# Optimization experiments

Hardware: AMD Instinct MI355X
Metric: run time of the kernel (lower is better)

The kernel has to match this reference:

```python
import jax, jax.numpy as jnp
import numpy as np
import math

IMAGE_SIZE = 256
VIEWING_ANGLE = 30.0  # degrees
NEAR = 0.1
FAR = 100.0
CHUNK = 50


def _look_at(vertices):
    # nr.look_at with at=origin, up=+y, eye from viewing_angle (as in __init__)
    eye = jnp.array([0.0, 0.0, -(1.0 / math.tan(math.radians(VIEWING_ANGLE)) + 1.0)],
                    dtype=vertices.dtype)
    at = jnp.zeros(3, dtype=vertices.dtype)
    up = jnp.array([0.0, 1.0, 0.0], dtype=vertices.dtype)
    z = at - eye
    z = z / jnp.linalg.norm(z)
    x = jnp.cross(up, z)
    x = x / jnp.linalg.norm(x)
    y = jnp.cross(z, x)
    y = y / jnp.linalg.norm(y)
    R = jnp.stack([x, y, z])  # [3,3] rows = camera axes
    return (vertices - eye) @ R.T


def _perspective(v):
    # nr.perspective: x,y divided by z*tan(angle); z (camera depth) kept
    width = math.tan(math.radians(VIEWING_ANGLE))
    z = v[..., 2]
    zs = jnp.where(jnp.abs(z) < 1e-5, 1e-5, z)  # avoid div-by-zero for behind-camera verts
    return jnp.stack([v[..., 0] / (zs * width), v[..., 1] / (zs * width), z], axis=-1)


def reference(vertices, faces):
    """Renderer.forward(vertices, faces, mode='depth'):
    fill_back -> look_at -> perspective -> vertices_to_faces -> rasterize_depth.
    Returns depth image [B, H, W] (FAR where no face covers the pixel)."""
    B = vertices.shape[0]
    # fill_back: append faces with reversed vertex order
    faces2 = jnp.concatenate([faces, faces[:, :, ::-1]], axis=1)  # [B, 2F, 3]
    v_scr = _perspective(_look_at(vertices))                      # [B, V, 3]
    # vertices_to_faces gather
    fv = jax.vmap(lambda v, f: v[f])(v_scr, faces2)               # [B, 2F, 3, 3]
    F2 = fv.shape[1]
    nsteps = F2 // CHUNK
    fv = fv.reshape(B, nsteps, CHUNK, 3, 3).transpose(1, 0, 2, 3, 4)  # [S,B,C,3,3]

    is_ = IMAGE_SIZE
    p = (2.0 * jnp.arange(is_, dtype=vertices.dtype) + 1.0 - is_) / is_  # pixel centers in (-1,1)
    py, px = jnp.meshgrid(p, p, indexing='ij')  # [H,W]

    def step(buf, f):  # f: [B,C,3,3]; z-buffer min over this face chunk
        x = f[..., 0][..., None, None]  # [B,C,3,1,1]
        y = f[..., 1][..., None, None]
        z = f[..., 2]                   # [B,C,3] camera-space depth per vertex
        x0, x1, x2 = x[:, :, 0], x[:, :, 1], x[:, :, 2]
        y0, y1, y2 = y[:, :, 0], y[:, :, 1], y[:, :, 2]
        area = (x1 - x0) * (y2 - y0) - (x2 - x0) * (y1 - y0)  # [B,C,1,1] signed 2*area
        area_s = jnp.where(jnp.abs(area) < 1e-8, 1e-8, area)
        # screen-space barycentric weights (edge functions / area)
        w0 = ((x1 - px) * (y2 - py) - (x2 - px) * (y1 - py)) / area_s
        w1 = ((x2 - px) * (y0 - py) - (x0 - px) * (y2 - py)) / area_s
        w2 = 1.0 - w0 - w1
        zc = jnp.maximum(z, 1e-4)  # safe for masked-out faces only
        # perspective-correct depth: z = 1 / (w0/z0 + w1/z1 + w2/z2)
        inv_z = (w0 / zc[:, :, 0, None, None] + w1 / zc[:, :, 1, None, None]
                 + w2 / zc[:, :, 2, None, None])
        zp = 1.0 / jnp.maximum(inv_z, 1e-6)
        front = jnp.all(z > NEAR, axis=-1)[..., None, None]
        inside = (w0 >= 0) & (w1 >= 0) & (w2 >= 0) & (jnp.abs(area) > 1e-8)
        valid = inside & front & (zp > NEAR) & (zp < FAR)
        zp = jnp.where(valid, zp, FAR)
        return jnp.minimum(buf, jnp.min(zp, axis=1)), None

    buf0 = jnp.full((B, is_, is_), FAR, dtype=vertices.dtype)
    depth, _ = jax.lax.scan(step, buf0, fv)
    return depth


def setup_inputs() -> dict:
    key = jax.random.key(0)
    kv, kf = jax.random.split(key)
    B, NV, NF = 1, 2502, 5000
    # mesh roughly within the camera frustum (eye at z~-2.73 looking at origin)
    vertices = 0.35 * jax.random.normal(kv, (B, NV, 3), dtype=jnp.float32)
    faces = jax.random.randint(kf, (B, NF, 3), 0, NV, dtype=jnp.int32)
    return {"vertices": vertices, "faces": faces}
```

## Files before the change

### kernel.cpp

```cpp
#include <hip/hip_runtime.h>

#define IS 256
#define NEARV 0.1f
#define FARV 100.0f
#define NTX 16
#define NTILES 256
#define SEGSZ 256
#define NSEGMAX 20
#define CAP (SEGSZ * NSEGMAX)
#define CHK 32
#define RBLOCKS 2048
#define RWAVES (RBLOCKS * 4)
#define NSLOTS (NTILES * 256)

__launch_bounds__(256)
__global__ void kprep(const float* __restrict__ verts, const int* __restrict__ faces,
                      float4* __restrict__ fd, int* __restrict__ cnt2,
                      unsigned short* __restrict__ list, unsigned int* __restrict__ zb,
                      int nf, int nseg) {
    __shared__ int scnt[NTILES];
    const int tid = threadIdx.x;
    const int bid = blockIdx.x;
    zb[bid * 256 + tid] = 0x42C80000u;
    if (bid >= nseg) return;

    scnt[tid] = 0;
    __syncthreads();

    const int f = bid * 256 + tid;
    int kx0 = 0, kx1 = -1, ky0 = 0, ky1 = -1;
    float bxmin = 0.f, bymin = 0.f, bxmax = -1.f, bymax = -1.f;
    if (f < nf) {
        int i0 = faces[f * 3 + 0];
        int i1 = faces[f * 3 + 1];
        int i2 = faces[f * 3 + 2];
        float z0 = verts[i0 * 3 + 2] + 2.7320508075688772f;
        float z1 = verts[i1 * 3 + 2] + 2.7320508075688772f;
        float z2 = verts[i2 * 3 + 2] + 2.7320508075688772f;
        bool front = (z0 > NEARV) && (z1 > NEARV) && (z2 > NEARV);
        float zs0 = (fabsf(z0) < 1e-5f) ? 1e-5f : z0;
        float zs1 = (fabsf(z1) < 1e-5f) ? 1e-5f : z1;
        float zs2 = (fabsf(z2) < 1e-5f) ? 1e-5f : z2;
        float d0 = zs0 * 0.57735026918962576f;
        float d1 = zs1 * 0.57735026918962576f;
        float d2 = zs2 * 0.57735026918962576f;
        float x0 = verts[i0 * 3 + 0] / d0;
        float y0 = verts[i0 * 3 + 1] / d0;
        float x1 = verts[i1 * 3 + 0] / d1;
        float y1 = verts[i1 * 3 + 1] / d1;
        float x2 = verts[i2 * 3 + 0] / d2;
        float y2 = verts[i2 * 3 + 1] / d2;
        float area = (x1 - x0) * (y2 - y0) - (x2 - x0) * (y1 - y0);
        if (front && (fabsf(area) > 1e-8f)) {
            bxmin = fminf(x0, fminf(x1, x2));
            bxmax = fmaxf(x0, fmaxf(x1, x2));
            bymin = fminf(y0, fminf(y1, y2));
            bymax = fmaxf(y0, fmaxf(y1, y2));
            float ia = 1.0f / area;
            float iz0 = 1.0f / fmaxf(z0, 1e-4f);
            float iz1 = 1.0f / fmaxf(z1, 1e-4f);
            float iz2 = 1.0f / fmaxf(z2, 1e-4f);
            float4* o = fd + (size_t)f * 4;
            o[0] = make_float4(x0, y0, x1, y1);
            o[1] = make_float4(x2, y2, ia, iz0);
            o[2] = make_float4(iz1, iz2, 0.0f, 0.0f);
            float tminx = fminf(fmaxf((bxmin * 256.0f + 225.0f) * (1.0f / 32.0f), -2.0f), 17.0f);
            float tmaxx = fminf(fmaxf((bxmax * 256.0f + 255.0f) * (1.0f / 32.0f), -2.0f), 17.0f);
            float tminy = fminf(fmaxf((bymin * 256.0f + 225.0f) * (1.0f / 32.0f), -2.0f), 17.0f);
            float tmaxy = fminf(fmaxf((bymax * 256.0f + 255.0f) * (1.0f / 32.0f), -2.0f), 17.0f);
            kx0 = max(0, (int)ceilf(tminx) - 1);
            kx1 = min(NTX - 1, (int)floorf(tmaxx) + 1);
            ky0 = max(0, (int)ceilf(tminy) - 1);
            ky1 = min(NTX - 1, (int)floorf(tmaxy) + 1);
        }
    }
    for (int ky = ky0; ky <= ky1; ++ky) {
        float py_lo = (float)(32 * ky - 255) * (1.0f / 256.0f);
        float py_hi = (float)(32 * ky - 225) * (1.0f / 256.0f);
        if (!(bymin <= py_hi && bymax >= py_lo)) continue;
        for (int kx = kx0; kx <= kx1; ++kx) {
            float px_lo = (float)(32 * kx - 255) * (1.0f / 256.0f);
            float px_hi = (float)(32 * kx - 225) * (1.0f / 256.0f);
            if (bxmin <= px_hi && bxmax >= px_lo) atomicAdd(&scnt[ky * NTX + kx], 1);
        }
    }
    __syncthreads();
    cnt2[tid * nseg + bid] = scnt[tid];
    scnt[tid] = 0;
    __syncthreads();
    for (int ky = ky0; ky <= ky1; ++ky) {
        float py_lo = (float)(32 * ky - 255) * (1.0f / 256.0f);
        float py_hi = (float)(32 * ky - 225) * (1.0f / 256.0f);
        if (!(bymin <= py_hi && bymax >= py_lo)) continue;
        for (int kx = kx0; kx <= kx1; ++kx) {
            float px_lo = (float)(32 * kx - 255) * (1.0f / 256.0f);
            float px_hi = (float)(32 * kx - 225) * (1.0f / 256.0f);
            if (bxmin <= px_hi && bxmax >= px_lo) {
                int t = ky * NTX + kx;
                int slot = atomicAdd(&scnt[t], 1);
                list[(size_t)t * CAP + bid * SEGSZ + slot] = (unsigned short)f;
            }
        }
    }
}

__launch_bounds__(256)
__global__ void kraster(const float4* __restrict__ fd, const unsigned short* __restrict__ list,
                        const int* __restrict__ cnt2, unsigned int* __restrict__ zb,
                        int nseg) {
    __shared__ float4 sdata[4][CHK * 3];
    const int wslot = __builtin_amdgcn_readfirstlane(threadIdx.x >> 6);
    const int wid = blockIdx.x * 4 + wslot;
    const int lane = threadIdx.x & 63;
    const int cx = lane & 15;
    const int ry = lane >> 4;
    float4* sd = &sdata[wslot][0];

    for (int w = wid; w < NSLOTS; w += RWAVES) {
        const int tile = w >> 8;
        const int slot = (w & 255) ^ tile;
        const int seg = slot >> 3;
        if (seg >= nseg) continue;
        const int c = cnt2[tile * nseg + seg];
        const int k = slot & 7;
        const int n0 = c - k * CHK;
        if (n0 <= 0) continue;
        const int n = min(CHK, n0);

        const int bx = tile & 15;
        const int by = tile >> 4;
        const int j = bx * 16 + cx;
        const float px = ((float)(2 * j + 1) - 256.0f) * (1.0f / 256.0f);
        float py[4];
        int row[4];
        unsigned int zcur[4];
#pragma unroll
        for (int r = 0; r < 4; ++r) {
            row[r] = by * 16 + ry + 4 * r;
            py[r] = ((float)(2 * row[r] + 1) - 256.0f) * (1.0f / 256.0f);
            zcur[r] = zb[row[r] * IS + j];
        }
        const unsigned short* lp = list + (size_t)tile * CAP + seg * SEGSZ + k * CHK;
        if (lane < n) {
            const int fidx = lp[lane];
            const float4* p = fd + (size_t)fidx * 4;
            float4 b0 = p[0];
            float4 b1 = p[1];
            float4 b2 = p[2];
            sd[lane * 3 + 0] = b0;
            sd[lane * 3 + 1] = b1;
            sd[lane * 3 + 2] = b2;
        }
        asm volatile("s_waitcnt lgkmcnt(0)" ::: "memory");

        float mx[4] = {0.0f, 0.0f, 0.0f, 0.0f};

#pragma unroll 2
        for (int e = 0; e < n; ++e) {
            float4 a0 = sd[e * 3 + 0];
            float4 a1 = sd[e * 3 + 1];
            float4 a2 = sd[e * 3 + 2];
            float dx0 = a0.x - px, dx1 = a0.z - px, dx2 = a1.x - px;
#pragma unroll
            for (int r = 0; r < 4; ++r) {
                float dy0 = a0.y - py[r], dy1 = a0.w - py[r], dy2 = a1.y - py[r];
                float e0 = dx1 * dy2 - dx2 * dy1;
                float e1 = dx2 * dy0 - dx0 * dy2;
                float w0 = e0 * a1.z;
                float w1 = e1 * a1.z;
                float w2 = 1.0f - w0 - w1;
                float invz = w0 * a1.w + w1 * a2.x + w2 * a2.y;
                float invzc = fmaxf(invz, 1e-6f);
                float wmin = fminf(fminf(w0, w1), w2);
                bool ok = (wmin >= 0.0f) && (invzc < 10.0f) && (invzc > 0.01f);
                if (ok) mx[r] = fmaxf(mx[r], invzc);
            }
        }
#pragma unroll
        for (int r = 0; r < 4; ++r) {
            if (mx[r] > 0.0f) {
                float zp = 1.0f / mx[r];
                unsigned int zbits = __float_as_uint(zp);
                if (zbits < zcur[r]) atomicMin(&zb[row[r] * IS + j], zbits);
            }
        }
    }
}

extern "C" void kernel_launch(void* const* d_in, const int* in_sizes, int n_in,
                              void* d_out, int out_size, void* d_ws, size_t ws_size,
                              hipStream_t stream) {
    const float* verts = (const float*)d_in[0];
    const int* faces = (const int*)d_in[1];
    unsigned int* zb = (unsigned int*)d_out;

    const int nf = in_sizes[1] / 3;
    const int nseg = (nf + SEGSZ - 1) / SEGSZ;

    char* ws = (char*)d_ws;
    size_t off = 0;
    float4* fd = (float4*)(ws + off);     off += (size_t)nf * 64;
    off = (off + 255) & ~(size_t)255;
    int* cnt2 = (int*)(ws + off);         off += (size_t)NTILES * NSEGMAX * 4;
    off = (off + 255) & ~(size_t)255;
    unsigned short* list = (unsigned short*)(ws + off);

    kprep<<<256, 256, 0, stream>>>(verts, faces, fd, cnt2, list, zb, nf, nseg);
    kraster<<<RBLOCKS, 256, 0, stream>>>(fd, list, cnt2, zb, nseg);
}
```

Baseline: 119.8 us.

## Use larger face segments and scrambled slot mapping for raster work balance

The binning kernel now runs 5 blocks of 1024 threads instead of 20 active blocks of 256. Each tile's face list is therefore split into fewer, larger segments, so the 32-face chunks handed to raster waves are fuller and there are fewer partial chunks and per-pixel atomics. The raster loop walks a fixed number of slots and maps each one through a multiplicative scramble, to spread busy tiles evenly across waves. The depth-buffer clear is vectorised to uint4 stores. In exchange, binning runs on only 5 CUs with more shared-atomic contention per block, and the segment count is hardcoded, capping input at 5120 faces.

```diff
diff --git a/kernel.cpp b/kernel.cpp
--- a/kernel.cpp
+++ b/kernel.cpp
@@ -5,29 +5,36 @@
 #define FARV 100.0f
 #define NTX 16
 #define NTILES 256
-#define SEGSZ 256
-#define NSEGMAX 20
-#define CAP (SEGSZ * NSEGMAX)
+#define SEGSZ 1024
+#define NSEG 5
+#define CAP (SEGSZ * NSEG)
 #define CHK 32
+#define KPS (SEGSZ / CHK)
+#define NSLOT (NTILES * NSEG * KPS)
 #define RBLOCKS 2048
 #define RWAVES (RBLOCKS * 4)
-#define NSLOTS (NTILES * 256)
-
-__launch_bounds__(256)
+#define SCRM 12347
+
+__launch_bounds__(SEGSZ)
 __global__ void kprep(const float* __restrict__ verts, const int* __restrict__ faces,
                       float4* __restrict__ fd, int* __restrict__ cnt2,
                       unsigned short* __restrict__ list, unsigned int* __restrict__ zb,
-                      int nf, int nseg) {
+                      int nf) {
     __shared__ int scnt[NTILES];
     const int tid = threadIdx.x;
     const int bid = blockIdx.x;
-    zb[bid * 256 + tid] = 0x42C80000u;
-    if (bid >= nseg) return;
-
-    scnt[tid] = 0;
+    const int gid = bid * SEGSZ + tid;
+
+    {
+        uint4* zb4 = (uint4*)zb;
+        const uint4 farv = make_uint4(0x42C80000u, 0x42C80000u, 0x42C80000u, 0x42C80000u);
+        for (int i = gid; i < (IS * IS) / 4; i += NSEG * SEGSZ) zb4[i] = farv;
+    }
+
+    if (tid < NTILES) scnt[tid] = 0;
     __syncthreads();
 
-    const int f = bid * 256 + tid;
+    const int f = gid;
     int kx0 = 0, kx1 = -1, ky0 = 0, ky1 = -1;
     float bxmin = 0.f, bymin = 0.f, bxmax = -1.f, bymax = -1.f;
     if (f < nf) {
@@ -85,8 +92,10 @@
         }
     }
     __syncthreads();
-    cnt2[tid * nseg + bid] = scnt[tid];
-    scnt[tid] = 0;
+    if (tid < NTILES) {
+        cnt2[tid * NSEG + bid] = scnt[tid];
+        scnt[tid] = 0;
+    }
     __syncthreads();
     for (int ky = ky0; ky <= ky1; ++ky) {
         float py_lo = (float)(32 * ky - 255) * (1.0f / 256.0f);
@@ -106,8 +115,7 @@
 
 __launch_bounds__(256)
 __global__ void kraster(const float4* __restrict__ fd, const unsigned short* __restrict__ list,
-                        const int* __restrict__ cnt2, unsigned int* __restrict__ zb,
-                        int nseg) {
+                        const int* __restrict__ cnt2, unsigned int* __restrict__ zb) {
     __shared__ float4 sdata[4][CHK * 3];
     const int wslot = __builtin_amdgcn_readfirstlane(threadIdx.x >> 6);
     const int wid = blockIdx.x * 4 + wslot;
@@ -116,13 +124,15 @@
     const int ry = lane >> 4;
     float4* sd = &sdata[wslot][0];
 
-    for (int w = wid; w < NSLOTS; w += RWAVES) {
-        const int tile = w >> 8;
-        const int slot = (w & 255) ^ tile;
-        const int seg = slot >> 3;
-        if (seg >= nseg) continue;
-        const int c = cnt2[tile * nseg + seg];
-        const int k = slot & 7;
+#pragma unroll 1
+    for (int i = 0; i < NSLOT / RWAVES; ++i) {
+        const int s = wid + i * RWAVES;
+        const int sp = (s * SCRM) % NSLOT;
+        const int tile = sp & 255;
+        const int rest = sp >> 8;
+        const int seg = rest >> 5;
+        const int k = rest & 31;
+        const int c = cnt2[tile * NSEG + seg];
         const int n0 = c - k * CHK;
         if (n0 <= 0) continue;
         const int n = min(CHK, n0);
@@ -195,16 +205,15 @@
     unsigned int* zb = (unsigned int*)d_out;
 
     const int nf = in_sizes[1] / 3;
-    const int nseg = (nf + SEGSZ - 1) / SEGSZ;
 
     char* ws = (char*)d_ws;
     size_t off = 0;
     float4* fd = (float4*)(ws + off);     off += (size_t)nf * 64;
     off = (off + 255) & ~(size_t)255;
-    int* cnt2 = (int*)(ws + off);         off += (size_t)NTILES * NSEGMAX * 4;
+    int* cnt2 = (int*)(ws + off);         off += (size_t)NTILES * NSEG * 4;
     off = (off + 255) & ~(size_t)255;
     unsigned short* list = (unsigned short*)(ws + off);
 
-    kprep<<<256, 256, 0, stream>>>(verts, faces, fd, cnt2, list, zb, nf, nseg);
-    kraster<<<RBLOCKS, 256, 0, stream>>>(fd, list, cnt2, zb, nseg);
+    kprep<<<NSEG, SEGSZ, 0, stream>>>(verts, faces, fd, cnt2, list, zb, nf);
+    kraster<<<RBLOCKS, 256, 0, stream>>>(fd, list, cnt2, zb);
 }
```

New measurement: 160.0 us. +33.5%, slower.
